# Kernel optimization log

Hardware: AMD Instinct MI355X
Metric: run time of the kernel (lower is better)

## Reference

```python
import jax, jax.numpy as jnp
import numpy as np

DIM = 512
HEADS = 8


def setup_inputs() -> dict:
    key = jax.random.key(0)
    k1, k2, k3, k4 = jax.random.split(key, 4)
    head_dim = DIM // HEADS
    scale = head_dim ** -0.5
    x = jax.random.normal(k1, (4, 4096, DIM), dtype=jnp.float32)
    Wqkv = jax.random.normal(k2, (3 * DIM, DIM), dtype=jnp.float32) * (DIM ** -0.5)
    temperature = jnp.ones((HEADS, 1, 1), dtype=jnp.float32) * scale
    Wproj = jax.random.normal(k3, (DIM, DIM), dtype=jnp.float32) * (DIM ** -0.5)
    bproj = jnp.zeros((DIM,), dtype=jnp.float32)
    return {"x": x, "Wqkv": Wqkv, "temperature": temperature, "Wproj": Wproj, "bproj": bproj}


def reference(x, Wqkv, temperature, Wproj, bproj):
    B, N, C = x.shape
    H = temperature.shape[0]
    D = C // H
    qkv = (x @ Wqkv.T).reshape(B, N, 3, H, D).transpose(2, 0, 3, 1, 4)  # (3,B,H,N,D)
    q, k, v = qkv[0], qkv[1], qkv[2]
    q = jax.nn.relu(q)
    k = jax.nn.relu(k)
    # denom = clamp(q @ sum_n k, min=100) -> (B,H,N,1)
    ksum = k.sum(axis=2)  # (B,H,D)
    denom = jnp.clip(jnp.einsum('bhnd,bhd->bhn', q, ksum), 100.0)[..., None]
    # attn = (k^T v) * temperature -> (B,H,D,D)
    attn = jnp.einsum('bhnd,bhne->bhde', k, v) * temperature
    attn1 = jnp.einsum('bhnd,bhde->bhne', q, attn)  # (B,H,N,D)
    out = attn1 / denom
    y = out.transpose(0, 2, 1, 3).reshape(B, N, C) @ Wproj.T + bproj
    return (y, attn1)
```

## Files before the change

### kernel.cpp

```cpp
#include <hip/hip_runtime.h>
#include <cstdint>
#include <cstddef>

typedef _Float16 f16;
typedef _Float16 f16x4 __attribute__((ext_vector_type(4)));
typedef _Float16 f16x8 __attribute__((ext_vector_type(8)));
typedef float f32x4 __attribute__((ext_vector_type(4)));

#define MFMA16(a, b, c) __builtin_amdgcn_mfma_f32_16x16x32_f16(a, b, c, 0, 0, 0)

static __device__ __forceinline__ void gld16(const void* g, void* l) {
  __builtin_amdgcn_global_load_lds(
      (const __attribute__((address_space(1))) void*)g,
      (__attribute__((address_space(3))) void*)l, 16, 0, 0);
}

#define B_ 4
#define N_ 4096
#define C_ 512
#define H_ 8
#define D_ 64
#define BN_ROWS 16384
#define QKV_COLS 1536

__global__ __launch_bounds__(256) void k_convert(
    const float* __restrict__ wqkv, const float* __restrict__ wproj,
    f16* __restrict__ wqkvh, f16* __restrict__ wprojh)
{
  const int NW1 = (QKV_COLS * C_) / 4;
  const int NW2 = (C_ * C_) / 4;
  const int total = NW1 + NW2;
  const int stride = gridDim.x * blockDim.x;
  for (int i = blockIdx.x * blockDim.x + threadIdx.x; i < total; i += stride) {
    const float4* s; f16x4* d; int j;
    if (i < NW1) { s = (const float4*)wqkv;  d = (f16x4*)wqkvh;  j = i; }
    else         { s = (const float4*)wproj; d = (f16x4*)wprojh; j = i - NW1; }
    float4 v = s[j];
    f16x4 o; o[0] = (f16)v.x; o[1] = (f16)v.y; o[2] = (f16)v.z; o[3] = (f16)v.w;
    d[j] = o;
  }
}

__global__ __launch_bounds__(256, 2) void k_qkv_gemm(
    const float* __restrict__ X, const f16* __restrict__ W, f16* __restrict__ Out)
{
  __shared__ f16 As[2][128][64];
  __shared__ f16 Bs[2][128][64];
  int w = (blockIdx.x & 7) * 192 + (blockIdx.x >> 3);
  const int m0 = (w / 12) * 128;
  const int n0 = (w % 12) * 128;
  const int tid = threadIdx.x;
  const int wid = tid >> 6, lane = tid & 63;
  const int lr = lane & 15, lg = lane >> 4;
  const int wm = wid >> 1, wn = wid & 1;
  const int sr = lane >> 3, sslot = (lane & 7) ^ sr;
  const int ar = tid >> 4;
  const int ac = tid & 15;
  const float* asrc = &X[(size_t)(m0 + ar) * 512 + ac * 4];
  float4 aregE[8], aregO[8];
  f32x4 acc[4][4] = {};

#define STAGE_B(tt, q)                                                        \
  do {                                                                        \
    _Pragma("unroll")                                                         \
    for (int i = 0; i < 4; ++i) {                                             \
      int chunk = wid * 4 + i;                                                \
      gld16(&W[(size_t)(n0 + chunk * 8 + sr) * 512 + (tt) * 64 + sslot * 8],  \
            &Bs[q][chunk * 8][0]);                                            \
    }                                                                         \
  } while (0)
#define LOADA(tt, set)                                                        \
  do {                                                                        \
    _Pragma("unroll")                                                         \
    for (int j = 0; j < 8; ++j)                                               \
      set[j] = *(const float4*)(asrc + (size_t)j * 16 * 512 + (tt) * 64);     \
  } while (0)
#define WRITEA(q, set)                                                        \
  do {                                                                        \
    _Pragma("unroll")                                                         \
    for (int j = 0; j < 8; ++j) {                                             \
      int row = j * 16 + ar;                                                  \
      int slot = ac >> 1;                                                     \
      f16x4 pk;                                                               \
      pk[0] = (f16)set[j].x; pk[1] = (f16)set[j].y;                           \
      pk[2] = (f16)set[j].z; pk[3] = (f16)set[j].w;                           \
      *(f16x4*)((char*)&As[q][row][0] + ((slot ^ (row & 7)) * 16 + (ac & 1) * 8)) = pk; \
    }                                                                         \
  } while (0)

  STAGE_B(0, 0);
  LOADA(0, aregE);
  asm volatile("s_waitcnt vmcnt(0)" ::: "memory");
  WRITEA(0, aregE);
  LOADA(1, aregO);
  asm volatile("s_waitcnt lgkmcnt(0)" ::: "memory");
  __builtin_amdgcn_s_barrier();
  asm volatile("" ::: "memory");

#pragma unroll
  for (int t = 0; t < 8; ++t) {
    const int p = t & 1, q = p ^ 1;
    if (t < 7) STAGE_B(t + 1, q);
    if (t < 6) {
      if ((t & 1) == 0) LOADA(t + 2, aregE); else LOADA(t + 2, aregO);
    }
    f16x8 af[2][4], bf[2][4];
#pragma unroll
    for (int kk = 0; kk < 2; ++kk) {
#pragma unroll
      for (int m = 0; m < 4; ++m)
        af[kk][m] = *(const f16x8*)&As[p][wm * 64 + m * 16 + lr][(((kk * 4 + lg) ^ (lr & 7)) * 8)];
#pragma unroll
      for (int n = 0; n < 4; ++n)
        bf[kk][n] = *(const f16x8*)&Bs[p][wn * 64 + n * 16 + lr][(((kk * 4 + lg) ^ (lr & 7)) * 8)];
    }
    if (t < 7) {
      if (t < 6) { asm volatile("s_waitcnt vmcnt(12)" ::: "memory"); }
      else       { asm volatile("s_waitcnt vmcnt(4)"  ::: "memory"); }
      if (((t + 1) & 1) == 0) WRITEA(q, aregE); else WRITEA(q, aregO);
    }
    asm volatile("s_waitcnt lgkmcnt(0)" ::: "memory");
    __builtin_amdgcn_sched_barrier(0);
    __builtin_amdgcn_s_setprio(1);
#pragma unroll
    for (int kk = 0; kk < 2; ++kk)
#pragma unroll
      for (int m = 0; m < 4; ++m)
#pragma unroll
        for (int n = 0; n < 4; ++n)
          acc[m][n] = MFMA16(bf[kk][n], af[kk][m], acc[m][n]);
    __builtin_amdgcn_s_setprio(0);
    if (t < 7) {
      if (t < 6) { asm volatile("s_waitcnt vmcnt(8)" ::: "memory"); }
      else       { asm volatile("s_waitcnt vmcnt(0)" ::: "memory"); }
      __builtin_amdgcn_s_barrier();
      asm volatile("" ::: "memory");
    }
  }
#undef STAGE_B
#undef LOADA
#undef WRITEA

  const bool relu = (n0 < 1024);
#pragma unroll
  for (int m = 0; m < 4; ++m)
#pragma unroll
    for (int n = 0; n < 4; ++n) {
      int row = m0 + wm * 64 + m * 16 + lr;
      int col = n0 + wn * 64 + n * 16 + lg * 4;
      f16x4 o;
#pragma unroll
      for (int j = 0; j < 4; ++j) {
        float v = acc[m][n][j];
        if (relu) v = fmaxf(v, 0.f);
        o[j] = (f16)v;
      }
      *(f16x4*)&Out[(size_t)row * QKV_COLS + col] = o;
    }
}

__global__ __launch_bounds__(256) void k_ktv(
    const f16* __restrict__ qkv, float* __restrict__ partial, float* __restrict__ pksum)
{
  __shared__ f16 ks[32][64];
  __shared__ f16 vs[32][64];
  const int bh = blockIdx.x, sp = blockIdx.y;
  const int b = bh >> 3, h = bh & 7;
  const int tid = threadIdx.x, wid = tid >> 6, lane = tid & 63;
  const int srow = lane >> 3, scol = (lane & 7) * 8;
  const int td = (wid << 2) | (lane >> 4);
  const int te = lane & 15;
  float acc[4][4] = {};
  float ksacc[4] = {0.f, 0.f, 0.f, 0.f};
  const size_t rowbase = (size_t)b * N_ + sp * 128;
  for (int t = 0; t < 4; ++t) {
    int nb = t * 32 + wid * 8 + srow;
    gld16(&qkv[(rowbase + nb) * QKV_COLS + 512 + h * 64 + scol], &ks[wid * 8][0]);
    gld16(&qkv[(rowbase + nb) * QKV_COLS + 1024 + h * 64 + scol], &vs[wid * 8][0]);
    __syncthreads();
#pragma unroll 4
    for (int n = 0; n < 32; ++n) {
      f16x4 kd = *(const f16x4*)&ks[n][td * 4];
      f16x4 ve = *(const f16x4*)&vs[n][te * 4];
      float kf[4], vf[4];
#pragma unroll
      for (int i = 0; i < 4; ++i) { kf[i] = (float)kd[i]; vf[i] = (float)ve[i]; }
#pragma unroll
      for (int i = 0; i < 4; ++i)
#pragma unroll
        for (int j = 0; j < 4; ++j)
          acc[i][j] += kf[i] * vf[j];
      if (te == 0) {
#pragma unroll
        for (int i = 0; i < 4; ++i) ksacc[i] += kf[i];
      }
    }
    __syncthreads();
  }
  float* pp = partial + (size_t)(bh * 32 + sp) * 4096;
#pragma unroll
  for (int i = 0; i < 4; ++i)
#pragma unroll
    for (int j = 0; j < 4; ++j)
      pp[(td * 4 + i) * 64 + te * 4 + j] = acc[i][j];
  if (te == 0) {
    float* kp = pksum + (bh * 32 + sp) * 64;
#pragma unroll
    for (int i = 0; i < 4; ++i) kp[td * 4 + i] = ksacc[i];
  }
}

__global__ __launch_bounds__(256) void k_reduce(
    const float* __restrict__ partial, const float* __restrict__ pksum,
    float* __restrict__ attn_acc, float* __restrict__ ksum)
{
  const int bh = blockIdx.x, seg = blockIdx.y, tid = threadIdx.x;
  const int i = seg * 256 + tid;
  float s = 0.f;
#pragma unroll 8
  for (int sp = 0; sp < 32; ++sp) s += partial[(size_t)(bh * 32 + sp) * 4096 + i];
  attn_acc[bh * 4096 + i] = s;
  if (seg == 0 && tid < 64) {
    float t2 = 0.f;
#pragma unroll 8
    for (int sp = 0; sp < 32; ++sp) t2 += pksum[(bh * 32 + sp) * 64 + tid];
    ksum[bh * 64 + tid] = t2;
  }
}

__global__ __launch_bounds__(256) void k_attn1(
    const f16* __restrict__ qkv, const float* __restrict__ attn_acc,
    const float* __restrict__ ksum, const float* __restrict__ temp,
    float* __restrict__ attn1_out, f16* __restrict__ outh)
{
  __shared__ f16 attnT[64][64];
  __shared__ float ksum_s[64];
  __shared__ float denom_s[256];
  const int bh = blockIdx.x, sp = blockIdx.y;
  const int b = bh >> 3, h = bh & 7;
  const int tid = threadIdx.x, wid = tid >> 6, lane = tid & 63;
  const int lr = lane & 15, lg = lane >> 4;
  const int n0 = sp * 256;
  const float tscale = temp[h];
  {
    int e = tid & 63, dblk = (tid >> 6) * 16;
    float vals[16];
#pragma unroll
    for (int x = 0; x < 16; ++x)
      vals[x] = attn_acc[bh * 4096 + (dblk + x) * 64 + e] * tscale;
#pragma unroll
    for (int half = 0; half < 2; ++half) {
      int slot = ((dblk >> 3) + half) ^ (e & 7);
      f16x8 pk;
#pragma unroll
      for (int j = 0; j < 8; ++j) pk[j] = (f16)vals[half * 8 + j];
      *(f16x8*)&attnT[e][slot * 8] = pk;
    }
  }
  if (tid < 64) ksum_s[tid] = ksum[bh * 64 + tid];
  __syncthreads();
  {
    size_t row = (size_t)b * N_ + n0 + tid;
    const f16* qrow = &qkv[row * QKV_COLS + h * 64];
    float dot = 0.f;
#pragma unroll
    for (int d0 = 0; d0 < 64; d0 += 8) {
      f16x8 qv = *(const f16x8*)&qrow[d0];
#pragma unroll
      for (int j = 0; j < 8; ++j) dot += (float)qv[j] * ksum_s[d0 + j];
    }
    denom_s[tid] = fmaxf(dot, 100.f);
  }
  f16x8 bf[4][2];
#pragma unroll
  for (int et = 0; et < 4; ++et)
#pragma unroll
    for (int kk = 0; kk < 2; ++kk) {
      int e = et * 16 + lr;
      bf[et][kk] = *(const f16x8*)&attnT[e][(((kk * 4 + lg) ^ (e & 7)) * 8)];
    }
  __syncthreads();
  f32x4 acc[4][4] = {};
#pragma unroll
  for (int mt = 0; mt < 4; ++mt) {
    size_t rbase = ((size_t)b * N_ + n0 + wid * 64 + mt * 16 + lr) * QKV_COLS + h * 64;
#pragma unroll
    for (int kk = 0; kk < 2; ++kk) {
      f16x8 a = *(const f16x8*)&qkv[rbase + kk * 32 + lg * 8];
#pragma unroll
      for (int et = 0; et < 4; ++et)
        acc[mt][et] = MFMA16(bf[et][kk], a, acc[mt][et]);
    }
  }
#pragma unroll
  for (int mt = 0; mt < 4; ++mt) {
    int rl = wid * 64 + mt * 16 + lr;
    int n = n0 + rl;
    float dn = denom_s[rl];
#pragma unroll
    for (int et = 0; et < 4; ++et) {
      int e = et * 16 + lg * 4;
      float4 o;
      f16x4 oh;
      o.x = acc[mt][et][0]; o.y = acc[mt][et][1]; o.z = acc[mt][et][2]; o.w = acc[mt][et][3];
#pragma unroll
      for (int j = 0; j < 4; ++j) oh[j] = (f16)(acc[mt][et][j] / dn);
      *(float4*)&attn1_out[((size_t)bh * N_ + n) * 64 + e] = o;
      *(f16x4*)&outh[((size_t)b * N_ + n) * 512 + h * 64 + e] = oh;
    }
  }
}

__global__ __launch_bounds__(256, 2) void k_proj_gemm(
    const f16* __restrict__ Xh, const f16* __restrict__ W,
    const float* __restrict__ bias, float* __restrict__ Y)
{
  __shared__ f16 As[2][128][64];
  __shared__ f16 Bs[2][128][64];
  int w = (blockIdx.x & 7) * 64 + (blockIdx.x >> 3);
  const int m0 = (w / 4) * 128;
  const int n0 = (w % 4) * 128;
  const int tid = threadIdx.x;
  const int wid = tid >> 6, lane = tid & 63;
  const int lr = lane & 15, lg = lane >> 4;
  const int wm = wid >> 1, wn = wid & 1;
  const int sr = lane >> 3, sslot = (lane & 7) ^ sr;
  f32x4 acc[4][4] = {};

#define STAGE8(tt, q)                                                         \
  do {                                                                        \
    _Pragma("unroll")                                                         \
    for (int i = 0; i < 4; ++i) {                                             \
      int chunk = wid * 4 + i;                                                \
      gld16(&Xh[(size_t)(m0 + chunk * 8 + sr) * 512 + (tt) * 64 + sslot * 8], \
            &As[q][chunk * 8][0]);                                            \
      gld16(&W[(size_t)(n0 + chunk * 8 + sr) * 512 + (tt) * 64 + sslot * 8],  \
            &Bs[q][chunk * 8][0]);                                            \
    }                                                                         \
  } while (0)

  STAGE8(0, 0);
  asm volatile("s_waitcnt vmcnt(0)" ::: "memory");
  __builtin_amdgcn_s_barrier();
  asm volatile("" ::: "memory");

#pragma unroll
  for (int t = 0; t < 8; ++t) {
    const int p = t & 1, q = p ^ 1;
    if (t < 7) STAGE8(t + 1, q);
    f16x8 af[2][4], bf[2][4];
#pragma unroll
    for (int kk = 0; kk < 2; ++kk) {
#pragma unroll
      for (int m = 0; m < 4; ++m)
        af[kk][m] = *(const f16x8*)&As[p][wm * 64 + m * 16 + lr][(((kk * 4 + lg) ^ (lr & 7)) * 8)];
#pragma unroll
      for (int n = 0; n < 4; ++n)
        bf[kk][n] = *(const f16x8*)&Bs[p][wn * 64 + n * 16 + lr][(((kk * 4 + lg) ^ (lr & 7)) * 8)];
    }
    asm volatile("s_waitcnt lgkmcnt(0)" ::: "memory");
    __builtin_amdgcn_sched_barrier(0);
    __builtin_amdgcn_s_setprio(1);
#pragma unroll
    for (int kk = 0; kk < 2; ++kk)
#pragma unroll
      for (int m = 0; m < 4; ++m)
#pragma unroll
        for (int n = 0; n < 4; ++n)
          acc[m][n] = MFMA16(bf[kk][n], af[kk][m], acc[m][n]);
    __builtin_amdgcn_s_setprio(0);
    if (t < 7) {
      asm volatile("s_waitcnt vmcnt(0)" ::: "memory");
      __builtin_amdgcn_s_barrier();
      asm volatile("" ::: "memory");
    }
  }
#undef STAGE8

#pragma unroll
  for (int m = 0; m < 4; ++m)
#pragma unroll
    for (int n = 0; n < 4; ++n) {
      int row = m0 + wm * 64 + m * 16 + lr;
      int col = n0 + wn * 64 + n * 16 + lg * 4;
      float4 o;
      o.x = acc[m][n][0] + bias[col + 0];
      o.y = acc[m][n][1] + bias[col + 1];
      o.z = acc[m][n][2] + bias[col + 2];
      o.w = acc[m][n][3] + bias[col + 3];
      *(float4*)&Y[(size_t)row * C_ + col] = o;
    }
}

extern "C" void kernel_launch(void* const* d_in, const int* in_sizes, int n_in,
                              void* d_out, int out_size, void* d_ws, size_t ws_size,
                              hipStream_t stream)
{
  const float* x     = (const float*)d_in[0];
  const float* wqkv  = (const float*)d_in[1];
  const float* temp  = (const float*)d_in[2];
  const float* wproj = (const float*)d_in[3];
  const float* bproj = (const float*)d_in[4];
  float* y_out     = (float*)d_out;
  float* attn1_out = (float*)d_out + 8388608;

  char* ws = (char*)d_ws;
  float* partial  = (float*)(ws);
  f16*   wqkvh    = (f16*)(ws + 16777216);
  f16*   wprojh   = (f16*)(ws + 18350080);
  f16*   qkvh     = (f16*)(ws + 18874368);
  float* attn_acc = (float*)(ws + 69206016);
  float* ksum     = (float*)(ws + 69730304);
  float* pksum    = (float*)(ws + 69738496);
  f16*   outh     = (f16*)(ws + 70000640);

  hipLaunchKernelGGL(k_convert,  dim3(256),     dim3(256), 0, stream, wqkv, wproj, wqkvh, wprojh);
  hipLaunchKernelGGL(k_qkv_gemm, dim3(1536),    dim3(256), 0, stream, x, wqkvh, qkvh);
  hipLaunchKernelGGL(k_ktv,      dim3(32, 32),  dim3(256), 0, stream, qkvh, partial, pksum);
  hipLaunchKernelGGL(k_reduce,   dim3(32, 16),  dim3(256), 0, stream, partial, pksum, attn_acc, ksum);
  hipLaunchKernelGGL(k_attn1,    dim3(32, 16),  dim3(256), 0, stream, qkvh, attn_acc, ksum, temp, attn1_out, outh);
  hipLaunchKernelGGL(k_proj_gemm,dim3(512),     dim3(256), 0, stream, outh, wprojh, bproj, y_out);
}
```

Baseline: 125.2 us.

## Stage fp32 X tiles directly into LDS and drop double-buffered pipeline

The QKV GEMM now loads fp32 X tiles straight into shared memory with direct global-to-LDS loads, using an XOR swizzle. It converts them to fp16 when reading MFMA fragments, instead of staging through registers and writing fp16 to LDS. The double-buffered register/LDS pipeline with hand-placed waitcnts is replaced by a single buffer and __syncthreads per K-step. This lowers register pressure and removes the register round-trip, but it loses the overlap of loads with MFMA and doubles the LDS footprint per A tile.

Result: no change. 126.3 us (+0.9%).

```diff
diff --git a/kernel.cpp b/kernel.cpp
--- a/kernel.cpp
+++ b/kernel.cpp
@@ -41,11 +41,11 @@
   }
 }
 
-__global__ __launch_bounds__(256, 2) void k_qkv_gemm(
+__global__ __launch_bounds__(256) void k_qkv_gemm(
     const float* __restrict__ X, const f16* __restrict__ W, f16* __restrict__ Out)
 {
-  __shared__ f16 As[2][128][64];
-  __shared__ f16 Bs[2][128][64];
+  __shared__ float Asf[128][64];
+  __shared__ f16   Bs[128][64];
   int w = (blockIdx.x & 7) * 192 + (blockIdx.x >> 3);
   const int m0 = (w / 12) * 128;
   const int n0 = (w % 12) * 128;
@@ -54,73 +54,44 @@
   const int lr = lane & 15, lg = lane >> 4;
   const int wm = wid >> 1, wn = wid & 1;
   const int sr = lane >> 3, sslot = (lane & 7) ^ sr;
-  const int ar = tid >> 4;
-  const int ac = tid & 15;
-  const float* asrc = &X[(size_t)(m0 + ar) * 512 + ac * 4];
-  float4 aregE[8], aregO[8];
+  const int ar4 = lane >> 4, aslot = lane & 15;
+  const int acolE = (aslot ^ ar4) * 4;
+  const int acolO = (aslot ^ (4 + ar4)) * 4;
   f32x4 acc[4][4] = {};
 
-#define STAGE_B(tt, q)                                                        \
-  do {                                                                        \
-    _Pragma("unroll")                                                         \
-    for (int i = 0; i < 4; ++i) {                                             \
-      int chunk = wid * 4 + i;                                                \
-      gld16(&W[(size_t)(n0 + chunk * 8 + sr) * 512 + (tt) * 64 + sslot * 8],  \
-            &Bs[q][chunk * 8][0]);                                            \
-    }                                                                         \
-  } while (0)
-#define LOADA(tt, set)                                                        \
-  do {                                                                        \
-    _Pragma("unroll")                                                         \
-    for (int j = 0; j < 8; ++j)                                               \
-      set[j] = *(const float4*)(asrc + (size_t)j * 16 * 512 + (tt) * 64);     \
-  } while (0)
-#define WRITEA(q, set)                                                        \
-  do {                                                                        \
-    _Pragma("unroll")                                                         \
-    for (int j = 0; j < 8; ++j) {                                             \
-      int row = j * 16 + ar;                                                  \
-      int slot = ac >> 1;                                                     \
-      f16x4 pk;                                                               \
-      pk[0] = (f16)set[j].x; pk[1] = (f16)set[j].y;                           \
-      pk[2] = (f16)set[j].z; pk[3] = (f16)set[j].w;                           \
-      *(f16x4*)((char*)&As[q][row][0] + ((slot ^ (row & 7)) * 16 + (ac & 1) * 8)) = pk; \
-    }                                                                         \
-  } while (0)
-
-  STAGE_B(0, 0);
-  LOADA(0, aregE);
-  asm volatile("s_waitcnt vmcnt(0)" ::: "memory");
-  WRITEA(0, aregE);
-  LOADA(1, aregO);
-  asm volatile("s_waitcnt lgkmcnt(0)" ::: "memory");
-  __builtin_amdgcn_s_barrier();
-  asm volatile("" ::: "memory");
-
-#pragma unroll
-  for (int t = 0; t < 8; ++t) {
-    const int p = t & 1, q = p ^ 1;
-    if (t < 7) STAGE_B(t + 1, q);
-    if (t < 6) {
-      if ((t & 1) == 0) LOADA(t + 2, aregE); else LOADA(t + 2, aregO);
-    }
+  for (int kt = 0; kt < 8; ++kt) {
+#pragma unroll
+    for (int i = 0; i < 8; ++i) {
+      int c = wid * 8 + i;
+      int row = c * 4 + ar4;
+      gld16(&X[(size_t)(m0 + row) * 512 + kt * 64 + ((c & 1) ? acolO : acolE)],
+            &Asf[c * 4][0]);
+    }
+#pragma unroll
+    for (int i = 0; i < 4; ++i) {
+      int chunk = wid * 4 + i;
+      gld16(&W[(size_t)(n0 + chunk * 8 + sr) * 512 + kt * 64 + sslot * 8],
+            &Bs[chunk * 8][0]);
+    }
+    __syncthreads();
     f16x8 af[2][4], bf[2][4];
 #pragma unroll
     for (int kk = 0; kk < 2; ++kk) {
 #pragma unroll
-      for (int m = 0; m < 4; ++m)
-        af[kk][m] = *(const f16x8*)&As[p][wm * 64 + m * 16 + lr][(((kk * 4 + lg) ^ (lr & 7)) * 8)];
+      for (int m = 0; m < 4; ++m) {
+        int row = wm * 64 + m * 16 + lr;
+        int s0 = kk * 8 + lg * 2;
+        f32x4 a0 = *(const f32x4*)((const char*)&Asf[row][0] + ((s0 ^ (row & 7)) * 16));
+        f32x4 a1 = *(const f32x4*)((const char*)&Asf[row][0] + (((s0 + 1) ^ (row & 7)) * 16));
+        f16x8 r;
+        r[0] = (f16)a0[0]; r[1] = (f16)a0[1]; r[2] = (f16)a0[2]; r[3] = (f16)a0[3];
+        r[4] = (f16)a1[0]; r[5] = (f16)a1[1]; r[6] = (f16)a1[2]; r[7] = (f16)a1[3];
+        af[kk][m] = r;
+      }
 #pragma unroll
       for (int n = 0; n < 4; ++n)
-        bf[kk][n] = *(const f16x8*)&Bs[p][wn * 64 + n * 16 + lr][(((kk * 4 + lg) ^ (lr & 7)) * 8)];
-    }
-    if (t < 7) {
-      if (t < 6) { asm volatile("s_waitcnt vmcnt(12)" ::: "memory"); }
-      else       { asm volatile("s_waitcnt vmcnt(4)"  ::: "memory"); }
-      if (((t + 1) & 1) == 0) WRITEA(q, aregE); else WRITEA(q, aregO);
-    }
-    asm volatile("s_waitcnt lgkmcnt(0)" ::: "memory");
-    __builtin_amdgcn_sched_barrier(0);
+        bf[kk][n] = *(const f16x8*)&Bs[wn * 64 + n * 16 + lr][(((kk * 4 + lg) ^ (lr & 7)) * 8)];
+    }
     __builtin_amdgcn_s_setprio(1);
 #pragma unroll
     for (int kk = 0; kk < 2; ++kk)
@@ -130,16 +101,8 @@
         for (int n = 0; n < 4; ++n)
           acc[m][n] = MFMA16(bf[kk][n], af[kk][m], acc[m][n]);
     __builtin_amdgcn_s_setprio(0);
-    if (t < 7) {
-      if (t < 6) { asm volatile("s_waitcnt vmcnt(8)" ::: "memory"); }
-      else       { asm volatile("s_waitcnt vmcnt(0)" ::: "memory"); }
-      __builtin_amdgcn_s_barrier();
-      asm volatile("" ::: "memory");
-    }
-  }
-#undef STAGE_B
-#undef LOADA
-#undef WRITEA
+    __syncthreads();
+  }
 
   const bool relu = (n0 < 1024);
 #pragma unroll
```
